# Performance work log

Hardware: AMD Instinct MI355X
Metric: run time of the kernel (lower is better)

The kernel has to match this reference:

```python
import jax, jax.numpy as jnp
import numpy as np

N_NODES = 40000
N_EDGES = 640000
D_IN = 128
D_HID = 128
D_OUT = 128
N_GRAPHS = 128


def setup_inputs() -> dict:
    key = jax.random.key(0)
    ks = jax.random.split(key, 12)
    x = jax.random.normal(ks[0], (N_NODES, D_IN), dtype=jnp.float32)
    edge_index = jax.random.randint(ks[1], (2, N_EDGES), 0, N_NODES, dtype=jnp.int64)
    batch = jnp.sort(jax.random.randint(ks[2], (N_NODES,), 0, N_GRAPHS, dtype=jnp.int64))
    def lin(k, fan_in, shape):
        s = 1.0 / np.sqrt(fan_in)
        return jax.random.uniform(k, shape, dtype=jnp.float32, minval=-s, maxval=s)
    return {
        "x": x, "edge_index": edge_index, "batch": batch,
        "W_rel0": lin(ks[3], D_IN, (D_IN, D_HID)), "b_rel0": lin(ks[4], D_IN, (D_HID,)), "W_root0": lin(ks[5], D_IN, (D_IN, D_HID)),
        "W_rel1": lin(ks[6], D_HID, (D_HID, D_HID)), "b_rel1": lin(ks[7], D_HID, (D_HID,)), "W_root1": lin(ks[8], D_HID, (D_HID, D_HID)),
        "W_rel2": lin(ks[9], D_HID, (D_HID, D_OUT)), "b_rel2": lin(ks[10], D_HID, (D_OUT,)), "W_root2": lin(ks[11], D_HID, (D_HID, D_OUT)),
    }


def graph_conv(x, src, dst, W_rel, b_rel, W_root):
    # PyG GraphConv: out_i = Lin_rel(sum_{j in N(i)} x_j) + Lin_root(x_i)
    agg = jax.ops.segment_sum(x[src], dst, num_segments=N_NODES)  # [N, F]
    return agg @ W_rel + b_rel + x @ W_root


def reference(x, edge_index, batch,
              W_rel0, b_rel0, W_root0,
              W_rel1, b_rel1, W_root1,
              W_rel2, b_rel2, W_root2):
    src, dst = edge_index[0], edge_index[1]
    h = graph_conv(x, src, dst, W_rel0, b_rel0, W_root0)
    h = jax.nn.relu(h)  # dropout is identity in eval mode
    h = graph_conv(h, src, dst, W_rel1, b_rel1, W_root1)
    h = jax.nn.relu(h)
    h = graph_conv(h, src, dst, W_rel2, b_rel2, W_root2)
    # global_max_pool over per-node graph ids -> [n_graphs, D_OUT]
    return jax.ops.segment_max(h, batch, num_segments=N_GRAPHS)
```

## Files before the change

### kernel.cpp

```cpp
#include <hip/hip_runtime.h>
#include <hip/hip_bf16.h>
#include <math.h>

#define N_NODES 40000
#define N_EDGES 640000
#define D 128
#define N_GRAPHS 128
#define SCAN_NBLK ((N_NODES + 255) / 256)
#define LDS_STRIDE 68

typedef __attribute__((ext_vector_type(8))) short bf16x8;
typedef __attribute__((ext_vector_type(4))) float f32x4;
typedef __attribute__((ext_vector_type(4))) unsigned int u32x4;

static __device__ __forceinline__ unsigned short f2b(float f) {
    unsigned int u = __float_as_uint(f);
    unsigned int r = (u + 0x7fffu + ((u >> 16) & 1u)) >> 16;
    return (unsigned short)r;
}
static __device__ __forceinline__ float blo(unsigned int u) {
    return __uint_as_float(u << 16);
}
static __device__ __forceinline__ float bhi(unsigned int u) {
    return __uint_as_float(u & 0xffff0000u);
}

__global__ void __launch_bounds__(256) k_init(
    const int* __restrict__ batch, int* __restrict__ counts,
    int* __restrict__ bounds,
    unsigned short* __restrict__ xb, unsigned short* __restrict__ hA,
    unsigned short* __restrict__ hB) {
    int n = blockIdx.x * 256 + threadIdx.x;
    if (n < N_NODES) {
        counts[n] = 0;
        int b = batch[n];
        if (n == 0) {
            for (int g = 0; g <= b; ++g) bounds[g] = 0;
        } else {
            int pb = batch[n - 1];
            for (int g = pb + 1; g <= b; ++g) bounds[g] = n;
        }
        if (n == N_NODES - 1) {
            for (int g = b + 1; g <= N_GRAPHS; ++g) bounds[g] = N_NODES;
        }
    }
    if (blockIdx.x == SCAN_NBLK) {
        int t = threadIdx.x;
        if (t < 48) {
            int row = t >> 4, c = t & 15;
            unsigned short* p = (row == 0) ? xb : (row == 1) ? hA : hB;
            u32x4 z = {0u, 0u, 0u, 0u};
            ((u32x4*)(p + (size_t)N_NODES * D))[c] = z;
        }
    }
}

__global__ void __launch_bounds__(256) k_pack1(
    const int* __restrict__ ei, int* __restrict__ counts,
    const float* __restrict__ x, unsigned int* __restrict__ xb,
    const float* __restrict__ Wr0, const float* __restrict__ Wt0,
    const float* __restrict__ Wr1, const float* __restrict__ Wt1,
    const float* __restrict__ Wr2, const float* __restrict__ Wt2,
    unsigned short* __restrict__ WT) {
    int b = blockIdx.x;
    int t = threadIdx.x;
    if (b < 2500) {
        int e = b * 256 + t;
        atomicAdd(&counts[ei[N_EDGES + e]], 1);
    } else if (b < 5000) {
        int i = (b - 2500) * 256 + t;
        const f32x4* xv = (const f32x4*)x;
        f32x4 v0 = xv[i * 2], v1 = xv[i * 2 + 1];
        u32x4 o;
        o.x = ((unsigned int)f2b(v0.y) << 16) | f2b(v0.x);
        o.y = ((unsigned int)f2b(v0.w) << 16) | f2b(v0.z);
        o.z = ((unsigned int)f2b(v1.y) << 16) | f2b(v1.x);
        o.w = ((unsigned int)f2b(v1.w) << 16) | f2b(v1.z);
        ((u32x4*)xb)[i] = o;
    } else {
        int bw = b - 5000;
        int l = bw >> 7, c = bw & 127, k = t;
        const float* Wrel = (l == 0) ? Wr0 : (l == 1) ? Wr1 : Wr2;
        const float* Wroot = (l == 0) ? Wt0 : (l == 1) ? Wt1 : Wt2;
        float v = (k < D) ? Wrel[k * D + c] : Wroot[(k - D) * D + c];
        WT[(size_t)l * 128 * 256 + c * 256 + k] = f2b(v);
    }
}

__global__ void __launch_bounds__(256) k_scan1(const int* __restrict__ counts,
                                               int* __restrict__ local_pre,
                                               int* __restrict__ blocksums) {
    int t = threadIdx.x;
    int i = blockIdx.x * 256 + t;
    int lane = t & 63, wave = t >> 6;
    int v = (i < N_NODES) ? ((counts[i] + 15) & ~15) : 0;
    int incl = v;
#pragma unroll
    for (int off = 1; off < 64; off <<= 1) {
        int u = __shfl_up(incl, off);
        if (lane >= off) incl += u;
    }
    __shared__ int ws[4];
    if (lane == 63) ws[wave] = incl;
    __syncthreads();
    int base = 0;
    for (int w = 0; w < 4; ++w) {
        int s = ws[w];
        if (w < wave) base += s;
    }
    if (i < N_NODES) local_pre[i] = base + incl - v;
    if (t == 255) blocksums[blockIdx.x] = base + incl;
}

__global__ void __launch_bounds__(256) k_scan2(int* __restrict__ blocksums) {
    int t = threadIdx.x;
    int lane = t & 63, wave = t >> 6;
    int v = (t < SCAN_NBLK) ? blocksums[t] : 0;
    int incl = v;
#pragma unroll
    for (int off = 1; off < 64; off <<= 1) {
        int u = __shfl_up(incl, off);
        if (lane >= off) incl += u;
    }
    __shared__ int ws[4];
    if (lane == 63) ws[wave] = incl;
    __syncthreads();
    int base = 0;
    for (int w = 0; w < 4; ++w) {
        int s = ws[w];
        if (w < wave) base += s;
    }
    if (t < SCAN_NBLK) blocksums[t] = base + incl - v;
}

__global__ void __launch_bounds__(256) k_scan3(const int* __restrict__ local_pre,
                                               const int* __restrict__ blocksums,
                                               const int* __restrict__ counts,
                                               int* __restrict__ rp_pad,
                                               int* __restrict__ cursor,
                                               int* __restrict__ src_pad) {
    int i = blockIdx.x * 256 + threadIdx.x;
    if (i < N_NODES) {
        int rp = blocksums[blockIdx.x] + local_pre[i];
        rp_pad[i] = rp;
        cursor[i] = rp;
        int c = counts[i];
        int pc = (c + 15) & ~15;
        for (int j = rp + c; j < rp + pc; ++j) src_pad[j] = N_NODES;
        if (i == N_NODES - 1) rp_pad[N_NODES] = rp + pc;
    }
}

__global__ void k_scatter(const int* __restrict__ ei, int* __restrict__ cursor,
                          int* __restrict__ src_pad) {
    int e = blockIdx.x * blockDim.x + threadIdx.x;
    if (e < N_EDGES) {
        int d = ei[N_EDGES + e];
        int pos = atomicAdd(&cursor[d], 1);
        src_pad[pos] = ei[e];
    }
}

__global__ void __launch_bounds__(256) k_layer(
    const unsigned short* __restrict__ in,
    const int* __restrict__ rp_pad,
    const int* __restrict__ src_pad,
    const unsigned short* __restrict__ WT,
    const float* __restrict__ bias,
    unsigned short* __restrict__ out,
    int relu) {
    __shared__ unsigned int aggLDS[16 * LDS_STRIDE];
    int tid = threadIdx.x;
    int w = tid >> 6;
    int lane = tid & 63;
    int q = lane >> 4;
    int c = lane & 15;
    int nl = w * 4 + q;
    int nodebase = blockIdx.x * 16;
    const u32x4* inv = (const u32x4*)in;

    int s = rp_pad[nodebase + nl];
    int e = rp_pad[nodebase + nl + 1];
    const int4* sidx = (const int4*)(src_pad + s);
    int ntrips = (e - s) >> 4;

    float a0 = 0.f, a1 = 0.f, a2 = 0.f, a3 = 0.f;
    float a4 = 0.f, a5 = 0.f, a6 = 0.f, a7 = 0.f;

#define ACC8(v) do { \
        a0 += blo((v).x); a1 += bhi((v).x); \
        a2 += blo((v).y); a3 += bhi((v).y); \
        a4 += blo((v).z); a5 += bhi((v).z); \
        a6 += blo((v).w); a7 += bhi((v).w); } while (0)

    for (int t = 0; t < ntrips; ++t) {
        int4 ia = sidx[4 * t + 0];
        int4 ib = sidx[4 * t + 1];
        int4 ic = sidx[4 * t + 2];
        int4 id = sidx[4 * t + 3];
        u32x4 v0 = inv[ia.x * 16 + c];
        u32x4 v1 = inv[ia.y * 16 + c];
        u32x4 v2 = inv[ia.z * 16 + c];
        u32x4 v3 = inv[ia.w * 16 + c];
        u32x4 v4 = inv[ib.x * 16 + c];
        u32x4 v5 = inv[ib.y * 16 + c];
        u32x4 v6 = inv[ib.z * 16 + c];
        u32x4 v7 = inv[ib.w * 16 + c];
        u32x4 v8 = inv[ic.x * 16 + c];
        u32x4 v9 = inv[ic.y * 16 + c];
        u32x4 va = inv[ic.z * 16 + c];
        u32x4 vb = inv[ic.w * 16 + c];
        u32x4 vc = inv[id.x * 16 + c];
        u32x4 vd = inv[id.y * 16 + c];
        u32x4 ve = inv[id.z * 16 + c];
        u32x4 vf = inv[id.w * 16 + c];
        ACC8(v0); ACC8(v1); ACC8(v2); ACC8(v3);
        ACC8(v4); ACC8(v5); ACC8(v6); ACC8(v7);
        ACC8(v8); ACC8(v9); ACC8(va); ACC8(vb);
        ACC8(vc); ACC8(vd); ACC8(ve); ACC8(vf);
    }
#undef ACC8

    u32x4 o;
    o.x = ((unsigned int)f2b(a1) << 16) | f2b(a0);
    o.y = ((unsigned int)f2b(a3) << 16) | f2b(a2);
    o.z = ((unsigned int)f2b(a5) << 16) | f2b(a4);
    o.w = ((unsigned int)f2b(a7) << 16) | f2b(a6);
    *(u32x4*)&aggLDS[nl * LDS_STRIDE + c * 4] = o;
    __syncthreads();

    int row = c, quad = q;
    int colbase = w * 32;

    f32x4 acc0 = {0.f, 0.f, 0.f, 0.f};
    f32x4 acc1 = {0.f, 0.f, 0.f, 0.f};

    const unsigned int* Al = &aggLDS[row * LDS_STRIDE];
    const short* Xp = (const short*)(in + (nodebase + row) * D);
    const short* W0 = (const short*)(WT + (colbase + row) * 256);
    const short* W1 = (const short*)(WT + (colbase + 16 + row) * 256);

#pragma unroll
    for (int t = 0; t < 4; ++t) {
        bf16x8 af = *(const bf16x8*)(Al + t * 16 + quad * 4);
        int k0 = t * 32 + quad * 8;
        bf16x8 b0 = *(const bf16x8*)(W0 + k0);
        bf16x8 b1 = *(const bf16x8*)(W1 + k0);
        acc0 = __builtin_amdgcn_mfma_f32_16x16x32_bf16(af, b0, acc0, 0, 0, 0);
        acc1 = __builtin_amdgcn_mfma_f32_16x16x32_bf16(af, b1, acc1, 0, 0, 0);
    }
#pragma unroll
    for (int t = 0; t < 4; ++t) {
        int k0 = t * 32 + quad * 8;
        bf16x8 xf = *(const bf16x8*)(Xp + k0);
        bf16x8 b0 = *(const bf16x8*)(W0 + 128 + k0);
        bf16x8 b1 = *(const bf16x8*)(W1 + 128 + k0);
        acc0 = __builtin_amdgcn_mfma_f32_16x16x32_bf16(xf, b0, acc0, 0, 0, 0);
        acc1 = __builtin_amdgcn_mfma_f32_16x16x32_bf16(xf, b1, acc1, 0, 0, 0);
    }

    int c0 = colbase + row, c1 = c0 + 16;
    float bia0 = bias[c0], bia1 = bias[c1];
#pragma unroll
    for (int r = 0; r < 4; ++r) {
        int n2 = nodebase + quad * 4 + r;
        float v0 = acc0[r] + bia0;
        float v1 = acc1[r] + bia1;
        if (relu) { v0 = fmaxf(v0, 0.f); v1 = fmaxf(v1, 0.f); }
        out[n2 * D + c0] = f2b(v0);
        out[n2 * D + c1] = f2b(v1);
    }
}

__global__ void __launch_bounds__(512) k_segmax(const unsigned short* __restrict__ h,
                                                const int* __restrict__ bounds,
                                                float* __restrict__ out) {
    __shared__ float sm[8][128];
    int g = blockIdx.x;
    int tid = threadIdx.x;
    int rg = tid >> 6;
    int c = tid & 63;
    int s = bounds[g], e = bounds[g + 1];
    const unsigned int* h32 = (const unsigned int*)h;

    float m0 = -INFINITY, m1 = -INFINITY;
    int n = s + rg;
    for (; n + 8 < e; n += 16) {
        unsigned int v0 = h32[n * 64 + c];
        unsigned int v1 = h32[(n + 8) * 64 + c];
        m0 = fmaxf(m0, blo(v0)); m1 = fmaxf(m1, bhi(v0));
        m0 = fmaxf(m0, blo(v1)); m1 = fmaxf(m1, bhi(v1));
    }
    if (n < e) {
        unsigned int v0 = h32[n * 64 + c];
        m0 = fmaxf(m0, blo(v0)); m1 = fmaxf(m1, bhi(v0));
    }
    sm[rg][c * 2] = m0;
    sm[rg][c * 2 + 1] = m1;
    __syncthreads();
    if (tid < 128) {
        float m = sm[0][tid];
#pragma unroll
        for (int r = 1; r < 8; ++r) m = fmaxf(m, sm[r][tid]);
        out[g * D + tid] = m;
    }
}

extern "C" void kernel_launch(void* const* d_in, const int* in_sizes, int n_in,
                              void* d_out, int out_size, void* d_ws, size_t ws_size,
                              hipStream_t stream) {
    const float* x = (const float*)d_in[0];
    const int* ei = (const int*)d_in[1];
    const int* batch = (const int*)d_in[2];
    const float* Wrel[3]  = {(const float*)d_in[3], (const float*)d_in[6], (const float*)d_in[9]};
    const float* brel[3]  = {(const float*)d_in[4], (const float*)d_in[7], (const float*)d_in[10]};
    const float* Wroot[3] = {(const float*)d_in[5], (const float*)d_in[8], (const float*)d_in[11]};
    float* out = (float*)d_out;

    char* ws = (char*)d_ws;
    size_t off = 0;
    auto alloc = [&](size_t bytes) -> void* {
        void* p = ws + off;
        off = (off + bytes + 255) & ~(size_t)255;
        return p;
    };
    unsigned short* xb  = (unsigned short*)alloc((size_t)(N_NODES + 1) * D * 2);
    unsigned short* hA  = (unsigned short*)alloc((size_t)(N_NODES + 1) * D * 2);
    unsigned short* hB  = (unsigned short*)alloc((size_t)(N_NODES + 1) * D * 2);
    unsigned short* WT  = (unsigned short*)alloc((size_t)3 * 128 * 256 * 2);
    int* rp_pad     = (int*)alloc((size_t)(N_NODES + 1) * 4);
    int* counts     = (int*)alloc((size_t)N_NODES * 4);
    int* cursor     = (int*)alloc((size_t)N_NODES * 4);
    int* src_pad    = (int*)alloc((size_t)(N_EDGES + 16 * N_NODES) * 4);
    int* bounds     = (int*)alloc((size_t)(N_GRAPHS + 1) * 4);
    int* local_pre  = (int*)alloc((size_t)N_NODES * 4);
    int* blocksums  = (int*)alloc((size_t)SCAN_NBLK * 4);

    k_init<<<SCAN_NBLK + 1, 256, 0, stream>>>(batch, counts, bounds, xb, hA, hB);
    k_pack1<<<5384, 256, 0, stream>>>(ei, counts, x, (unsigned int*)xb,
                                      Wrel[0], Wroot[0], Wrel[1], Wroot[1],
                                      Wrel[2], Wroot[2], WT);
    k_scan1<<<SCAN_NBLK, 256, 0, stream>>>(counts, local_pre, blocksums);
    k_scan2<<<1, 256, 0, stream>>>(blocksums);
    k_scan3<<<SCAN_NBLK, 256, 0, stream>>>(local_pre, blocksums, counts,
                                           rp_pad, cursor, src_pad);
    k_scatter<<<(N_EDGES + 255) / 256, 256, 0, stream>>>(ei, cursor, src_pad);

    const unsigned short* in = xb;
    unsigned short* houts[3] = {hA, hB, hA};
    for (int l = 0; l < 3; ++l) {
        k_layer<<<N_NODES / 16, 256, 0, stream>>>(in, rp_pad, src_pad,
                                                  WT + (size_t)l * 128 * 256,
                                                  brel[l], houts[l], (l < 2) ? 1 : 0);
        in = houts[l];
    }

    k_segmax<<<N_GRAPHS, 512, 0, stream>>>(houts[2], bounds, out);
}
```

Measured before the change: 281.6 us.

## Fuse global max pool into last layer via ordered-key atomicMax; prefetch root operands

The last GraphConv layer now reduces its outputs straight into the per-graph max, using atomicMax on order-preserving integer keys held in the output buffer. A small unmap kernel then converts the keys back to floats. This removes the separate segmax kernel and the write and reread of the final hidden matrix. The layer kernel also loads the root-input and rel-weight fragments before the gather loop so their latency overlaps the aggregation. The cost is atomic contention on the 128x128 output and an extra tiny launch.

```diff
diff --git a/kernel.cpp b/kernel.cpp
--- a/kernel.cpp
+++ b/kernel.cpp
@@ -24,13 +24,18 @@
 static __device__ __forceinline__ float bhi(unsigned int u) {
     return __uint_as_float(u & 0xffff0000u);
 }
+static __device__ __forceinline__ unsigned int fkey(float x) {
+    unsigned int b = __float_as_uint(x);
+    return (b & 0x80000000u) ? ~b : (b | 0x80000000u);
+}
 
 __global__ void __launch_bounds__(256) k_init(
     const int* __restrict__ batch, int* __restrict__ counts,
     int* __restrict__ bounds,
     unsigned short* __restrict__ xb, unsigned short* __restrict__ hA,
-    unsigned short* __restrict__ hB) {
+    unsigned short* __restrict__ hB, unsigned int* __restrict__ outk) {
     int n = blockIdx.x * 256 + threadIdx.x;
+    if (n < N_GRAPHS * D) outk[n] = 0x007FFFFFu;
     if (n < N_NODES) {
         counts[n] = 0;
         int b = batch[n];
@@ -168,7 +173,8 @@
     const unsigned short* __restrict__ WT,
     const float* __restrict__ bias,
     unsigned short* __restrict__ out,
-    int relu) {
+    const int* __restrict__ batch,
+    unsigned int* __restrict__ outk) {
     __shared__ unsigned int aggLDS[16 * LDS_STRIDE];
     int tid = threadIdx.x;
     int w = tid >> 6;
@@ -178,6 +184,20 @@
     int nl = w * 4 + q;
     int nodebase = blockIdx.x * 16;
     const u32x4* inv = (const u32x4*)in;
+
+    int row = c, quad = q;
+    int colbase = w * 32;
+    const short* Xp = (const short*)(in + (nodebase + row) * D);
+    const short* W0 = (const short*)(WT + (colbase + row) * 256);
+    const short* W1 = (const short*)(WT + (colbase + 16 + row) * 256);
+    bf16x8 xf[4], b0a[4], b1a[4];
+#pragma unroll
+    for (int t = 0; t < 4; ++t) {
+        int k0 = t * 32 + quad * 8;
+        xf[t] = *(const bf16x8*)(Xp + k0);
+        b0a[t] = *(const bf16x8*)(W0 + k0);
+        b1a[t] = *(const bf16x8*)(W1 + k0);
+    }
 
     int s = rp_pad[nodebase + nl];
     int e = rp_pad[nodebase + nl + 1];
@@ -229,81 +249,66 @@
     *(u32x4*)&aggLDS[nl * LDS_STRIDE + c * 4] = o;
     __syncthreads();
 
-    int row = c, quad = q;
-    int colbase = w * 32;
-
     f32x4 acc0 = {0.f, 0.f, 0.f, 0.f};
     f32x4 acc1 = {0.f, 0.f, 0.f, 0.f};
-
     const unsigned int* Al = &aggLDS[row * LDS_STRIDE];
-    const short* Xp = (const short*)(in + (nodebase + row) * D);
-    const short* W0 = (const short*)(WT + (colbase + row) * 256);
-    const short* W1 = (const short*)(WT + (colbase + 16 + row) * 256);
 
 #pragma unroll
     for (int t = 0; t < 4; ++t) {
         bf16x8 af = *(const bf16x8*)(Al + t * 16 + quad * 4);
-        int k0 = t * 32 + quad * 8;
-        bf16x8 b0 = *(const bf16x8*)(W0 + k0);
-        bf16x8 b1 = *(const bf16x8*)(W1 + k0);
-        acc0 = __builtin_amdgcn_mfma_f32_16x16x32_bf16(af, b0, acc0, 0, 0, 0);
-        acc1 = __builtin_amdgcn_mfma_f32_16x16x32_bf16(af, b1, acc1, 0, 0, 0);
+        acc0 = __builtin_amdgcn_mfma_f32_16x16x32_bf16(af, b0a[t], acc0, 0, 0, 0);
+        acc1 = __builtin_amdgcn_mfma_f32_16x16x32_bf16(af, b1a[t], acc1, 0, 0, 0);
     }
 #pragma unroll
     for (int t = 0; t < 4; ++t) {
         int k0 = t * 32 + quad * 8;
-        bf16x8 xf = *(const bf16x8*)(Xp + k0);
         bf16x8 b0 = *(const bf16x8*)(W0 + 128 + k0);
         bf16x8 b1 = *(const bf16x8*)(W1 + 128 + k0);
-        acc0 = __builtin_amdgcn_mfma_f32_16x16x32_bf16(xf, b0, acc0, 0, 0, 0);
-        acc1 = __builtin_amdgcn_mfma_f32_16x16x32_bf16(xf, b1, acc1, 0, 0, 0);
+        acc0 = __builtin_amdgcn_mfma_f32_16x16x32_bf16(xf[t], b0, acc0, 0, 0, 0);
+        acc1 = __builtin_amdgcn_mfma_f32_16x16x32_bf16(xf[t], b1, acc1, 0, 0, 0);
     }
 
     int c0 = colbase + row, c1 = c0 + 16;
     float bia0 = bias[c0], bia1 = bias[c1];
-#pragma unroll
-    for (int r = 0; r < 4; ++r) {
-        int n2 = nodebase + quad * 4 + r;
-        float v0 = acc0[r] + bia0;
-        float v1 = acc1[r] + bia1;
-        if (relu) { v0 = fmaxf(v0, 0.f); v1 = fmaxf(v1, 0.f); }
-        out[n2 * D + c0] = f2b(v0);
-        out[n2 * D + c1] = f2b(v1);
-    }
-}
-
-__global__ void __launch_bounds__(512) k_segmax(const unsigned short* __restrict__ h,
-                                                const int* __restrict__ bounds,
-                                                float* __restrict__ out) {
-    __shared__ float sm[8][128];
-    int g = blockIdx.x;
-    int tid = threadIdx.x;
-    int rg = tid >> 6;
-    int c = tid & 63;
-    int s = bounds[g], e = bounds[g + 1];
-    const unsigned int* h32 = (const unsigned int*)h;
-
-    float m0 = -INFINITY, m1 = -INFINITY;
-    int n = s + rg;
-    for (; n + 8 < e; n += 16) {
-        unsigned int v0 = h32[n * 64 + c];
-        unsigned int v1 = h32[(n + 8) * 64 + c];
-        m0 = fmaxf(m0, blo(v0)); m1 = fmaxf(m1, bhi(v0));
-        m0 = fmaxf(m0, blo(v1)); m1 = fmaxf(m1, bhi(v1));
-    }
-    if (n < e) {
-        unsigned int v0 = h32[n * 64 + c];
-        m0 = fmaxf(m0, blo(v0)); m1 = fmaxf(m1, bhi(v0));
-    }
-    sm[rg][c * 2] = m0;
-    sm[rg][c * 2 + 1] = m1;
-    __syncthreads();
-    if (tid < 128) {
-        float m = sm[0][tid];
-#pragma unroll
-        for (int r = 1; r < 8; ++r) m = fmaxf(m, sm[r][tid]);
-        out[g * D + tid] = m;
-    }
+    float v0[4], v1[4];
+#pragma unroll
+    for (int r = 0; r < 4; ++r) { v0[r] = acc0[r] + bia0; v1[r] = acc1[r] + bia1; }
+
+    if (outk == nullptr) {
+#pragma unroll
+        for (int r = 0; r < 4; ++r) {
+            int n2 = nodebase + quad * 4 + r;
+            out[n2 * D + c0] = f2b(fmaxf(v0[r], 0.f));
+            out[n2 * D + c1] = f2b(fmaxf(v1[r], 0.f));
+        }
+    } else {
+        int g0 = batch[nodebase];
+        int g15 = batch[nodebase + 15];
+        if (g0 == g15) {
+            float m0 = fmaxf(fmaxf(v0[0], v0[1]), fmaxf(v0[2], v0[3]));
+            float m1 = fmaxf(fmaxf(v1[0], v1[1]), fmaxf(v1[2], v1[3]));
+            m0 = fmaxf(m0, __shfl_xor(m0, 16)); m0 = fmaxf(m0, __shfl_xor(m0, 32));
+            m1 = fmaxf(m1, __shfl_xor(m1, 16)); m1 = fmaxf(m1, __shfl_xor(m1, 32));
+            if (quad == 0) {
+                atomicMax(&outk[g0 * D + c0], fkey(m0));
+                atomicMax(&outk[g0 * D + c1], fkey(m1));
+            }
+        } else {
+#pragma unroll
+            for (int r = 0; r < 4; ++r) {
+                int gg = batch[nodebase + quad * 4 + r];
+                atomicMax(&outk[gg * D + c0], fkey(v0[r]));
+                atomicMax(&outk[gg * D + c1], fkey(v1[r]));
+            }
+        }
+    }
+}
+
+__global__ void k_unmap(unsigned int* __restrict__ outk) {
+    int i = blockIdx.x * 256 + threadIdx.x;
+    unsigned int k = outk[i];
+    unsigned int b = (k & 0x80000000u) ? (k ^ 0x80000000u) : ~k;
+    ((float*)outk)[i] = __uint_as_float(b);
 }
 
 extern "C" void kernel_launch(void* const* d_in, const int* in_sizes, int n_in,
@@ -315,7 +320,7 @@
     const float* Wrel[3]  = {(const float*)d_in[3], (const float*)d_in[6], (const float*)d_in[9]};
     const float* brel[3]  = {(const float*)d_in[4], (const float*)d_in[7], (const float*)d_in[10]};
     const float* Wroot[3] = {(const float*)d_in[5], (const float*)d_in[8], (const float*)d_in[11]};
-    float* out = (float*)d_out;
+    unsigned int* outk = (unsigned int*)d_out;
 
     char* ws = (char*)d_ws;
     size_t off = 0;
@@ -336,7 +341,7 @@
     int* local_pre  = (int*)alloc((size_t)N_NODES * 4);
     int* blocksums  = (int*)alloc((size_t)SCAN_NBLK * 4);
 
-    k_init<<<SCAN_NBLK + 1, 256, 0, stream>>>(batch, counts, bounds, xb, hA, hB);
+    k_init<<<SCAN_NBLK + 1, 256, 0, stream>>>(batch, counts, bounds, xb, hA, hB, outk);
     k_pack1<<<5384, 256, 0, stream>>>(ei, counts, x, (unsigned int*)xb,
                                       Wrel[0], Wroot[0], Wrel[1], Wroot[1],
                                       Wrel[2], Wroot[2], WT);
@@ -346,14 +351,12 @@
                                            rp_pad, cursor, src_pad);
     k_scatter<<<(N_EDGES + 255) / 256, 256, 0, stream>>>(ei, cursor, src_pad);
 
-    const unsigned short* in = xb;
-    unsigned short* houts[3] = {hA, hB, hA};
-    for (int l = 0; l < 3; ++l) {
-        k_layer<<<N_NODES / 16, 256, 0, stream>>>(in, rp_pad, src_pad,
-                                                  WT + (size_t)l * 128 * 256,
-                                                  brel[l], houts[l], (l < 2) ? 1 : 0);
-        in = houts[l];
-    }
-
-    k_segmax<<<N_GRAPHS, 512, 0, stream>>>(houts[2], bounds, out);
-}
+    k_layer<<<N_NODES / 16, 256, 0, stream>>>(xb, rp_pad, src_pad, WT,
+                                              brel[0], hA, batch, nullptr);
+    k_layer<<<N_NODES / 16, 256, 0, stream>>>(hA, rp_pad, src_pad, WT + 128 * 256,
+                                              brel[1], hB, batch, nullptr);
+    k_layer<<<N_NODES / 16, 256, 0, stream>>>(hB, rp_pad, src_pad, WT + 2 * 128 * 256,
+                                              brel[2], hB, batch, outk);
+
+    k_unmap<<<N_GRAPHS * D / 256, 256, 0, stream>>>(outk);
+}
```

After: 276.1 us. Within noise of the previous version (-2.0%).
